# Performance work log

Measured on AMD Instinct MI355X. Metric: run time of the kernel, lower is better.

## Reference

```python
import jax, jax.numpy as jnp
import numpy as np

BLOCK_SIZE = 128
N_OUT = 4096
K_IN = 4096


def setup_inputs() -> dict:
    key = jax.random.key(0)
    k_x, k_w, k_s = jax.random.split(key, 3)
    x = jax.random.normal(k_x, (1, 1024, K_IN), dtype=jnp.float32)
    # ternary weights stored as int8 in {-2,-1,0,+1} (zero-point subtracted)
    weight_q = (jax.random.randint(k_w, (N_OUT, K_IN), 0, 4) - 2).astype(jnp.int8)
    n_blocks = K_IN // BLOCK_SIZE
    scales = jax.random.uniform(k_s, (N_OUT, n_blocks), dtype=jnp.float32) * 0.1 + 0.01
    return {"x": x, "weight_q": weight_q, "scales": scales}


def reference(x, weight_q, scales):
    N, K = weight_q.shape
    n_blocks = K // BLOCK_SIZE
    orig_shape = x.shape
    # [tokens, n_blocks, block_size]
    x_blocked = x.reshape(-1, n_blocks, BLOCK_SIZE).astype(jnp.float32)
    # [N, n_blocks, block_size]
    w_blocked = weight_q.reshape(N, n_blocks, BLOCK_SIZE).astype(jnp.float32)
    # per-block partial dot products: [tokens, N, n_blocks]
    raw = jnp.einsum('bki,nki->bnk', x_blocked, w_blocked)
    # apply per-(out_feature, block) scale then reduce over blocks
    out = (raw * scales).sum(axis=-1)  # [tokens, N]
    return out.astype(x.dtype).reshape(*orig_shape[:-1], N)
```

## Files before the change

kernel.cpp:

```cpp
#include <hip/hip_runtime.h>
#include <stdint.h>


#define MM 1024
#define NN 4096
#define KK 4096
#define BK 128

typedef __attribute__((ext_vector_type(4))) int intx4;
typedef __attribute__((ext_vector_type(4))) float floatx4;

typedef const __attribute__((address_space(1))) void global_cvoid;
typedef __attribute__((address_space(3))) void lds_void;

__global__ __launch_bounds__(256) void prep(const float* __restrict__ x,
                                            const int* __restrict__ wq,
                                            char* __restrict__ xq,
                                            float* __restrict__ qrow,
                                            char* __restrict__ wb) {
    const int tid = threadIdx.x;
    if (blockIdx.x < MM) {
        const int m = blockIdx.x;
        const float* xr = x + (size_t)m * KK;
        floatx4 v[4];
        float amax = 0.f;
#pragma unroll
        for (int c = 0; c < 4; ++c) {
            v[c] = *(const floatx4*)(xr + (c * 256 + tid) * 4);
#pragma unroll
            for (int e = 0; e < 4; ++e) amax = fmaxf(amax, fabsf(v[c][e]));
        }
#pragma unroll
        for (int off = 32; off; off >>= 1) amax = fmaxf(amax, __shfl_down(amax, off));
        __shared__ float wmax[4];
        if ((tid & 63) == 0) wmax[tid >> 6] = amax;
        __syncthreads();
        amax = fmaxf(fmaxf(wmax[0], wmax[1]), fmaxf(wmax[2], wmax[3]));
        amax = fmaxf(amax, 1e-20f);
        const float qinv = 127.0f / amax;
        if (tid == 0) qrow[m] = amax / 127.0f;
#pragma unroll
        for (int c = 0; c < 4; ++c) {
            int p = 0;
#pragma unroll
            for (int e = 0; e < 4; ++e) {
                float r = rintf(v[c][e] * qinv);
                r = fminf(fmaxf(r, -127.f), 127.f);
                p |= ((int)r & 255) << (8 * e);
            }
            *(int*)(xq + (size_t)m * KK + (c * 256 + tid) * 4) = p;
        }
    } else {
        const int blk = blockIdx.x - MM;
#pragma unroll
        for (int c = 0; c < 4; ++c) {
            size_t c4 = (size_t)blk * 1024 + c * 256 + tid;
            intx4 a = ((const intx4*)wq)[c4];
            ((int*)wb)[c4] = (a[0] & 255) | ((a[1] & 255) << 8) |
                             ((a[2] & 255) << 16) | (a[3] << 24);
        }
    }
}

__global__ __launch_bounds__(256, 2) void q8_gemm(const char* __restrict__ xq,
                                                  const char* __restrict__ wb,
                                                  const float* __restrict__ qrow,
                                                  const float* __restrict__ scales,
                                                  float* __restrict__ out) {
    __shared__ char As[2][64 * BK];
    __shared__ char Bs[2][128 * BK];
    __shared__ float Sl[128 * 33];

    const int tid  = threadIdx.x;
    const int lane = tid & 63;
    const int wave = tid >> 6;
    const int r16  = lane & 15;
    const int quad = lane >> 4;
    const int sw   = r16 & 7;
    const int wn   = wave * 32;

    const int bid = blockIdx.x;
    const int xcd = bid & 7, loc = bid >> 3;
    const int nT = xcd * 4 + (loc & 3);
    const int mT = loc >> 2;
    const int mBase = mT * 64, nBase = nT * 128;

    const int rg = lane >> 3;
    const int cs = (lane & 7) ^ rg;
    const char* gA = xq + (size_t)(mBase + wave * 16 + rg) * KK + cs * 16;
    const char* gB = wb + (size_t)(nBase + wave * 32 + rg) * KK + cs * 16;
    const int ldsRowA = wave * 16;
    const int ldsRowB = wave * 32;

    floatx4 facc[4][2];
#pragma unroll
    for (int i = 0; i < 4; ++i)
#pragma unroll
        for (int j = 0; j < 2; ++j) facc[i][j] = (floatx4){0.f, 0.f, 0.f, 0.f};

#define STAGE(BUF, SLAB)                                                        \
    {                                                                           \
        _Pragma("unroll")                                                       \
        for (int t = 0; t < 2; ++t)                                             \
            __builtin_amdgcn_global_load_lds(                                   \
                (global_cvoid*)(gA + (size_t)(t * 8) * KK + (SLAB) * BK),       \
                (lds_void*)&As[BUF][(ldsRowA + t * 8) * BK], 16, 0, 0);         \
        _Pragma("unroll")                                                       \
        for (int t = 0; t < 4; ++t)                                             \
            __builtin_amdgcn_global_load_lds(                                   \
                (global_cvoid*)(gB + (size_t)(t * 8) * KK + (SLAB) * BK),       \
                (lds_void*)&Bs[BUF][(ldsRowB + t * 8) * BK], 16, 0, 0);         \
    }

#define COMPUTE(BUF, SLAB)                                                      \
    {                                                                           \
        float sf0 = Sl[(wn + r16) * 33 + (SLAB)];                               \
        float sf1 = Sl[(wn + 16 + r16) * 33 + (SLAB)];                          \
        intx4 iacc[4][2];                                                       \
        _Pragma("unroll")                                                       \
        for (int kp = 0; kp < 2; ++kp) {                                        \
            intx4 av[4], bv[2];                                                 \
            _Pragma("unroll")                                                   \
            for (int i = 0; i < 4; ++i)                                         \
                av[i] = *(const intx4*)&As[BUF][(i * 16 + r16) * BK +           \
                                               (((kp * 4 + quad) ^ sw) << 4)];  \
            _Pragma("unroll")                                                   \
            for (int j = 0; j < 2; ++j)                                         \
                bv[j] = *(const intx4*)&Bs[BUF][(wn + j * 16 + r16) * BK +      \
                                               (((kp * 4 + quad) ^ sw) << 4)];  \
            _Pragma("unroll")                                                   \
            for (int i = 0; i < 4; ++i)                                         \
                _Pragma("unroll")                                               \
                for (int j = 0; j < 2; ++j)                                     \
                    iacc[i][j] = __builtin_amdgcn_mfma_i32_16x16x64_i8(         \
                        av[i], bv[j], kp ? iacc[i][j] : (intx4){0, 0, 0, 0},    \
                        0, 0, 0);                                               \
        }                                                                       \
        _Pragma("unroll")                                                       \
        for (int i = 0; i < 4; ++i)                                             \
            _Pragma("unroll")                                                   \
            for (int r = 0; r < 4; ++r) {                                       \
                facc[i][0][r] += (float)iacc[i][0][r] * sf0;                    \
                facc[i][1][r] += (float)iacc[i][1][r] * sf1;                    \
            }                                                                   \
    }

    STAGE(0, 0)
    for (int t = tid; t < 4096; t += 256) {
        int nl = t >> 5, b = t & 31;
        Sl[nl * 33 + b] = scales[(size_t)(nBase + nl) * 32 + b];
    }
    __syncthreads();

    const int NIT = KK / BK;
    for (int it = 0; it < NIT; it += 2) {
        if (it + 1 < NIT) STAGE(1, it + 1)
        COMPUTE(0, it)
        __syncthreads();
        if (it + 2 < NIT) STAGE(0, it + 2)
        COMPUTE(1, it + 1)
        __syncthreads();
    }

#pragma unroll
    for (int i = 0; i < 4; ++i) {
        floatx4 qv = *(const floatx4*)(qrow + mBase + i * 16 + quad * 4);
#pragma unroll
        for (int r = 0; r < 4; ++r) {
            int mg = mBase + i * 16 + quad * 4 + r;
            float* orow = out + (size_t)mg * NN + nBase + wn + r16;
#pragma unroll
            for (int j = 0; j < 2; ++j) orow[j * 16] = facc[i][j][r] * qv[r];
        }
    }
#undef STAGE
#undef COMPUTE
}

extern "C" void kernel_launch(void* const* d_in, const int* in_sizes, int n_in,
                              void* d_out, int out_size, void* d_ws, size_t ws_size,
                              hipStream_t stream) {
    const float* x      = (const float*)d_in[0];
    const int*   wq     = (const int*)d_in[1];
    const float* scales = (const float*)d_in[2];
    float*       out    = (float*)d_out;

    char*  xq   = (char*)d_ws;
    float* qrow = (float*)((char*)d_ws + (size_t)MM * KK);
    char*  wb   = (char*)d_ws + (size_t)MM * KK + 4096;

    prep<<<MM + (size_t)NN * KK / 16 / 256, 256, 0, stream>>>(x, wq, xq, qrow, wb);
    q8_gemm<<<(MM / 64) * (NN / 128), 256, 0, stream>>>(xq, wb, qrow, scales, out);
}
```

Before: 141.7 us.

## Split K in two across blocks with atomic accumulation and bf16 scales

Splits the K dimension into two halves, doubling the grid so each block handles 16 slabs and adds its partial result into a zeroed output with float atomics. Scales are stored in LDS as bf16 to cut shared memory, and launch bounds are raised to allow three blocks per CU. This aims to improve occupancy and fill more CUs. In exchange it adds a memset, atomic traffic on the output and nondeterministic summation order, and rounding the scales to bf16 reduces precision.

```diff
diff --git a/kernel.cpp b/kernel.cpp
--- a/kernel.cpp
+++ b/kernel.cpp
@@ -12,6 +12,15 @@
 
 typedef const __attribute__((address_space(1))) void global_cvoid;
 typedef __attribute__((address_space(3))) void lds_void;
+
+__device__ __forceinline__ unsigned short f2bf(float f) {
+    union { float f; unsigned u; } v; v.f = f;
+    return (unsigned short)((v.u + 0x7FFFu + ((v.u >> 16) & 1u)) >> 16);
+}
+__device__ __forceinline__ float bf2f(unsigned short b) {
+    union { unsigned u; float f; } v; v.u = ((unsigned)b) << 16;
+    return v.f;
+}
 
 __global__ __launch_bounds__(256) void prep(const float* __restrict__ x,
                                             const int* __restrict__ wq,
@@ -62,14 +71,14 @@
     }
 }
 
-__global__ __launch_bounds__(256, 2) void q8_gemm(const char* __restrict__ xq,
+__global__ __launch_bounds__(256, 3) void q8_gemm(const char* __restrict__ xq,
                                                   const char* __restrict__ wb,
                                                   const float* __restrict__ qrow,
                                                   const float* __restrict__ scales,
                                                   float* __restrict__ out) {
     __shared__ char As[2][64 * BK];
     __shared__ char Bs[2][128 * BK];
-    __shared__ float Sl[128 * 33];
+    __shared__ unsigned short Sl[128 * 17];
 
     const int tid  = threadIdx.x;
     const int lane = tid & 63;
@@ -82,8 +91,10 @@
     const int bid = blockIdx.x;
     const int xcd = bid & 7, loc = bid >> 3;
     const int nT = xcd * 4 + (loc & 3);
-    const int mT = loc >> 2;
+    const int mT = (loc >> 2) & 15;
+    const int kh = loc >> 6;
     const int mBase = mT * 64, nBase = nT * 128;
+    const int sl0 = kh * 16;
 
     const int rg = lane >> 3;
     const int cs = (lane & 7) ^ rg;
@@ -112,10 +123,10 @@
                 (lds_void*)&Bs[BUF][(ldsRowB + t * 8) * BK], 16, 0, 0);         \
     }
 
-#define COMPUTE(BUF, SLAB)                                                      \
+#define COMPUTE(BUF, SLOC)                                                      \
     {                                                                           \
-        float sf0 = Sl[(wn + r16) * 33 + (SLAB)];                               \
-        float sf1 = Sl[(wn + 16 + r16) * 33 + (SLAB)];                          \
+        float sf0 = bf2f(Sl[(wn + r16) * 17 + (SLOC)]);                         \
+        float sf1 = bf2f(Sl[(wn + 16 + r16) * 17 + (SLOC)]);                    \
         intx4 iacc[4][2];                                                       \
         _Pragma("unroll")                                                       \
         for (int kp = 0; kp < 2; ++kp) {                                        \
@@ -145,19 +156,18 @@
             }                                                                   \
     }
 
-    STAGE(0, 0)
-    for (int t = tid; t < 4096; t += 256) {
-        int nl = t >> 5, b = t & 31;
-        Sl[nl * 33 + b] = scales[(size_t)(nBase + nl) * 32 + b];
+    STAGE(0, sl0)
+    for (int t = tid; t < 2048; t += 256) {
+        int nl = t >> 4, b = t & 15;
+        Sl[nl * 17 + b] = f2bf(scales[(size_t)(nBase + nl) * 32 + sl0 + b]);
     }
     __syncthreads();
 
-    const int NIT = KK / BK;
-    for (int it = 0; it < NIT; it += 2) {
-        if (it + 1 < NIT) STAGE(1, it + 1)
+    for (int it = 0; it < 16; it += 2) {
+        if (it + 1 < 16) STAGE(1, sl0 + it + 1)
         COMPUTE(0, it)
         __syncthreads();
-        if (it + 2 < NIT) STAGE(0, it + 2)
+        if (it + 2 < 16) STAGE(0, sl0 + it + 2)
         COMPUTE(1, it + 1)
         __syncthreads();
     }
@@ -170,7 +180,8 @@
             int mg = mBase + i * 16 + quad * 4 + r;
             float* orow = out + (size_t)mg * NN + nBase + wn + r16;
 #pragma unroll
-            for (int j = 0; j < 2; ++j) orow[j * 16] = facc[i][j][r] * qv[r];
+            for (int j = 0; j < 2; ++j)
+                unsafeAtomicAdd(&orow[j * 16], facc[i][j][r] * qv[r]);
         }
     }
 #undef STAGE
@@ -189,6 +200,7 @@
     float* qrow = (float*)((char*)d_ws + (size_t)MM * KK);
     char*  wb   = (char*)d_ws + (size_t)MM * KK + 4096;
 
+    hipMemsetAsync(d_out, 0, (size_t)out_size * sizeof(float), stream);
     prep<<<MM + (size_t)NN * KK / 16 / 256, 256, 0, stream>>>(x, wq, xq, qrow, wb);
-    q8_gemm<<<(MM / 64) * (NN / 128), 256, 0, stream>>>(xq, wb, qrow, scales, out);
-}
+    q8_gemm<<<2 * (MM / 64) * (NN / 128), 256, 0, stream>>>(xq, wb, qrow, scales, out);
+}
```

Measured after the change: 374.8 us. +164.5%, slower.
